# Performance work log

Hardware: AMD Instinct MI355X
Metric: run time of the kernel (lower is better)

## Reference

```python
import jax, jax.numpy as jnp
import numpy as np

B, N, C = 64, 8192, 64
C4 = C // 4
EPS_BN = 1e-5


def setup_inputs() -> dict:
    key = jax.random.key(0)
    ks = jax.random.split(key, 12)
    s = 0.05
    return {
        "x": jax.random.normal(ks[0], (B, N, 10), jnp.float32),
        "y": jax.random.normal(ks[1], (B, N, 13), jnp.float32),
        "W_l": jax.random.normal(ks[2], (10, C), jnp.float32) * s,
        "b_l": jax.random.normal(ks[3], (C,), jnp.float32) * s,
        "W_r": jax.random.normal(ks[4], (13, C), jnp.float32) * s,
        "b_r": jax.random.normal(ks[5], (C,), jnp.float32) * s,
        "W_qk": jax.random.normal(ks[6], (C4, C), jnp.float32) * s,  # shared q/k 1x1-conv weight
        "W_v": jax.random.normal(ks[7], (C, C), jnp.float32) * s,
        "b_v": jax.random.normal(ks[8], (C,), jnp.float32) * s,
        "W_t": jax.random.normal(ks[9], (C, C), jnp.float32) * s,
        "b_t": jax.random.normal(ks[10], (C,), jnp.float32) * s,
        "gamma": jnp.ones((C,), jnp.float32),
        "beta": jnp.zeros((C,), jnp.float32),
    }


def reference(x, y, W_l, b_l, W_r, b_r, W_qk, W_v, b_v, W_t, b_t, gamma, beta):
    # x: [B,N,10] -> linear_l; y: [B,N,13] -> linear_r  (torch keeps [B,C,N]; we keep [B,N,C])
    X = x @ W_l + b_l                                   # [B,N,C]
    Y = y @ W_r + b_r                                   # [B,N,C]
    # 1x1 convs == per-point matmuls; attention runs ACROSS the batch dim per point n
    xq = jnp.einsum('bnc,dc->nbd', X, W_qk)             # [N,B,C/4]
    yk = jnp.einsum('bnc,dc->nbd', Y, W_qk)             # [N,B,C/4] (shared weight)
    yv = jnp.einsum('bnc,dc->nbd', Y, W_v) + b_v        # [N,B,C]
    energy = jnp.einsum('nbd,ned->nbe', xq, yk)         # [N,B,B]
    attn = jax.nn.softmax(energy, axis=-1)
    # extra L1 renormalization over dim=1 (offset-attention style)
    attn = attn / (1e-9 + attn.sum(axis=1, keepdims=True))
    yr = jnp.einsum('nbe,nec->bnc', attn, yv)           # [B,N,C]
    # trans_conv -> BatchNorm (training-mode batch stats) -> ReLU -> residual -> max over points
    t = jnp.einsum('bnc,dc->bnd', X - yr, W_t) + b_t    # [B,N,C]
    mean = t.mean(axis=(0, 1))
    var = t.var(axis=(0, 1))                            # biased var, as BN uses
    tn = gamma * (t - mean) * jax.lax.rsqrt(var + EPS_BN) + beta
    xres = X + jax.nn.relu(tn)                          # [B,N,C]
    return jnp.max(xres, axis=1)[:, :, None]            # [B,C,1] to match torch layout
```

## Files before the change

kernel.cpp:

```cpp
#include <hip/hip_runtime.h>

#define B_ 64
#define N_ 8192

using short8 = __attribute__((ext_vector_type(8))) short;
using f32x4  = __attribute__((ext_vector_type(4))) float;

#define MFMA16(a, b, c) __builtin_amdgcn_mfma_f32_16x16x32_bf16((a), (b), (c), 0, 0, 0)

__device__ inline unsigned short f2bf(float f) {
  union { float f; unsigned int u; } v; v.f = f;
  return (unsigned short)((v.u + 0x8000u) >> 16);
}
__device__ inline float bf2f(unsigned int hi16_in_low) {
  union { unsigned int u; float f; } v; v.u = hi16_in_low << 16;
  return v.f;
}
__device__ inline unsigned u2(float a, float b) {
  return (unsigned)f2bf(a) | ((unsigned)f2bf(b) << 16);
}
__device__ inline void put_y(short* Ar0, short* YT0, int b, int f, unsigned short h) {
  const int s = (f >= 13) ? 1 : 0;
  Ar0[16 + f + 2547 * s] = (short)h;
  YT0[f * 72 + b + 216 * s] = (short)h;
}


__global__ void k0_prep(const float* __restrict__ W_l, const float* __restrict__ b_l,
                        const float* __restrict__ W_r, const float* __restrict__ b_r,
                        const float* __restrict__ W_qk, const float* __restrict__ W_v,
                        const float* __restrict__ b_v, const float* __restrict__ W_t,
                        float* __restrict__ wsf) {
  const int tid = threadIdx.x;
  unsigned short* wb   = (unsigned short*)(wsf + 66688);
  unsigned short* BM   = wb;
  unsigned short* BL   = wb + 512;
  unsigned short* BRV2 = wb + 2560;
  unsigned short* BT   = wb + 4608;
  if (blockIdx.x == 0) {
    __shared__ float Wlq[11 * 16], Wrk[14 * 16];
    for (int idx = tid; idx < 11 * 16; idx += 256) {
      int i = idx >> 4, d = idx & 15;
      const float* a = (i < 10) ? (W_l + i * 64) : b_l;
      float s = 0.f;
      for (int c = 0; c < 64; ++c) s = fmaf(a[c], W_qk[d * 64 + c], s);
      Wlq[idx] = s;
    }
    for (int idx = tid; idx < 14 * 16; idx += 256) {
      int j = idx >> 4, d = idx & 15;
      const float* a = (j < 13) ? (W_r + j * 64) : b_r;
      float s = 0.f;
      for (int c = 0; c < 64; ++c) s = fmaf(a[c], W_qk[d * 64 + c], s);
      Wrk[idx] = s;
    }
    __syncthreads();
    for (int idx = tid; idx < 512; idx += 256) {
      int j = idx >> 5, kk = idx & 31;
      unsigned short o = 0;
      if (j < 14 && kk < 11) {
        float s = 0.f;
        for (int d = 0; d < 16; ++d) s = fmaf(Wlq[kk * 16 + d], Wrk[j * 16 + d], s);
        o = f2bf(s);
      }
      BM[idx] = o;
    }
  } else if (blockIdx.x == 1) {
    for (int idx = tid; idx < 2048; idx += 256) {
      int c = idx >> 5, kk = idx & 31;
      unsigned short o = 0;
      if (kk < 13) {
        float s = 0.f;
        for (int j = 0; j < 64; ++j) s = fmaf(W_r[kk * 64 + j], W_v[c * 64 + j], s);
        o = f2bf(s);
      } else if (kk == 13) {
        float s = b_v[c];
        for (int j = 0; j < 64; ++j) s = fmaf(b_r[j], W_v[c * 64 + j], s);
        o = f2bf(s);
      }
      BRV2[idx] = o;
    }
  } else if (blockIdx.x == 2) {
    for (int idx = tid; idx < 2048; idx += 256) {
      int c = idx >> 5, kk = idx & 31;
      unsigned short o = 0;
      if (kk < 10) o = f2bf(W_l[kk * 64 + c]);
      else if (kk == 10) o = f2bf(b_l[c]);
      BL[idx] = o;
    }
    for (int i = tid; i < 1024; i += 256) wsf[i] = 0.f;
  } else {
    for (int i = tid; i < 4096; i += 256) BT[i] = f2bf(W_t[i]);
  }
}

__global__ __launch_bounds__(256, 4)
void k1_attn(const float* __restrict__ x, const float* __restrict__ y,
             const float* __restrict__ wsf, const float* __restrict__ b_t,
             float* __restrict__ stats) {
  __shared__ __align__(16) short lds[19712];
  float* const statsScr = (float*)lds;
  short* const Axy[2] = {lds, lds + 2560};
  short* const YTb[2] = {lds + 5120, lds + 6272};
  short* const awB    = lds + 7424;
  short* const guB    = lds + 16640;
  float* const csF    = (float*)(lds + 18688);

  const unsigned short* wb   = (const unsigned short*)(wsf + 66688);
  const unsigned short* BM   = wb;
  const unsigned short* BL   = wb + 512;
  const unsigned short* BRV2 = wb + 2560;
  const unsigned short* BT   = wb + 4608;
  unsigned short* tg = (unsigned short*)(wsf + 66688) + 8704;

  const int tid  = threadIdx.x;
  const int w    = tid >> 6;
  const int lane = tid & 63;
  const int l15  = lane & 15;
  const int q    = lane >> 4;
  const int r0   = w * 16;
  const int n0   = blockIdx.x * 2;
  short* const aw[2] = {awB + w * 1152, awB + (4 + w) * 1152};
  short* const gu[2] = {guB + w * 256,  guB + (4 + w) * 256};

  {
    const int b = tid >> 2, i = tid & 3;
    const float* xb = x + ((size_t)b * N_ + n0) * 10;
    const float* yb = y + ((size_t)b * N_ + n0) * 13;
    short* const Ar0 = Axy[0] + b * 40;
    short* const Ar1 = Axy[1] + b * 40;
    short* const YT0 = YTb[0];
    {
      const float4 v = *(const float4*)(xb + 4 * i);
      const int g0 = 4 * i, g1 = 4 * i + 2;
      *(unsigned*)(Ar0 + (g0 >= 10 ? g0 + 2550 : g0)) = u2(v.x, v.y);
      *(unsigned*)(Ar0 + (g1 >= 10 ? g1 + 2550 : g1)) = u2(v.z, v.w);
      if (i == 0) {
        const float4 vv = *(const float4*)(xb + 16);
        *(unsigned*)(Ar1 + 6) = u2(vv.x, vv.y);
        *(unsigned*)(Ar1 + 8) = u2(vv.z, vv.w);
      }
    }
    if (i == 1) { *(unsigned*)(Ar1 + 10) = 0x3F80u; *(unsigned*)(Ar1 + 12) = 0u; *(unsigned*)(Ar1 + 14) = 0u; }
    if (i == 2) { *(unsigned*)(Ar0 + 10) = 0x3F80u; *(unsigned*)(Ar0 + 12) = 0u; *(unsigned*)(Ar0 + 14) = 0u; }
#pragma unroll
    for (int t = 0; t < 3; ++t) {
      const int j = i + 4 * t;
      const float2 v = *(const float2*)(yb + 2 * j);
      put_y(Ar0, YT0, b, 2 * j,     f2bf(v.x));
      put_y(Ar0, YT0, b, 2 * j + 1, f2bf(v.y));
    }
    if (i == 0) {
      const float2 v = *(const float2*)(yb + 24);
      put_y(Ar0, YT0, b, 24, f2bf(v.x));
      put_y(Ar0, YT0, b, 25, f2bf(v.y));
    }
    if (i == 3) {
      Ar0[29] = (short)0x3F80; *(unsigned*)(Ar0 + 30) = 0u;
      YT0[13 * 72 + b] = (short)0x3F80; YT0[14 * 72 + b] = 0; YT0[15 * 72 + b] = 0;
    }
    if (i == 2) {
      Ar1[29] = (short)0x3F80; *(unsigned*)(Ar1 + 30) = 0u;
      short* YT1 = YT0 + 1152;
      YT1[13 * 72 + b] = (short)0x3F80; YT1[14 * 72 + b] = 0; YT1[15 * 72 + b] = 0;
    }
  }
  asm volatile("s_waitcnt lgkmcnt(0)" ::: "memory");
  __builtin_amdgcn_sched_barrier(0);

  const short8 z8 = {0, 0, 0, 0, 0, 0, 0, 0};
  const f32x4 zero4 = {0.f, 0.f, 0.f, 0.f};

  const short8 bmF = *(const short8*)&BM[l15 * 32 + q * 8];
  short8 blF[4];
#pragma unroll
  for (int f = 0; f < 4; ++f) blF[f] = *(const short8*)&BL[(f * 16 + l15) * 32 + q * 8];

  f32x4 X[2][4];
  __builtin_amdgcn_s_setprio(1);
#pragma unroll
  for (int p = 0; p < 2; ++p) {
    const short8 aA = *(const short8*)&Axy[p][(r0 + l15) * 40 + q * 8];
    f32x4 G = MFMA16(aA, bmF, zero4);
#pragma unroll
    for (int f = 0; f < 4; ++f) X[p][f] = MFMA16(aA, blF[f], zero4);
#pragma unroll
    for (int j = 0; j < 4; ++j) gu[p][(q * 4 + j) * 16 + l15] = (short)f2bf(G[j]);
  }
  __builtin_amdgcn_s_setprio(0);
  __syncthreads();

  f32x4 E[2][4];
  __builtin_amdgcn_s_setprio(1);
#pragma unroll
  for (int p = 0; p < 2; ++p) {
    short8 aG = z8;
    if (q < 2) aG = *(const short8*)&gu[p][l15 * 16 + q * 8];
#pragma unroll
    for (int f = 0; f < 4; ++f) {
      short8 bk = z8;
      if (q < 2) bk = *(const short8*)&Axy[p][(f * 16 + l15) * 40 + 16 + q * 8];
      E[p][f] = MFMA16(aG, bk, zero4);
    }
  }
  __builtin_amdgcn_s_setprio(0);

  float inv_r[2][4];
#pragma unroll
  for (int p = 0; p < 2; ++p)
#pragma unroll
    for (int j = 0; j < 4; ++j) {
      float s = 0.f;
#pragma unroll
      for (int f = 0; f < 4; ++f) { E[p][f][j] = __expf(E[p][f][j]); s += E[p][f][j]; }
      s += __shfl_xor(s, 1);
      s += __shfl_xor(s, 2);
      s += __shfl_xor(s, 4);
      s += __shfl_xor(s, 8);
      inv_r[p][j] = 1.0f / s;
    }
#pragma unroll
  for (int p = 0; p < 2; ++p)
#pragma unroll
    for (int f = 0; f < 4; ++f) {
      float cs = E[p][f][0] * inv_r[p][0] + E[p][f][1] * inv_r[p][1] +
                 E[p][f][2] * inv_r[p][2] + E[p][f][3] * inv_r[p][3];
      cs += __shfl_xor(cs, 16);
      cs += __shfl_xor(cs, 32);
      if (lane < 16) csF[p * 256 + w * 64 + f * 16 + l15] = cs;
    }
  __syncthreads();

#pragma unroll
  for (int p = 0; p < 2; ++p) {
#pragma unroll
    for (int f = 0; f < 4; ++f) {
      const int col = f * 16 + l15;
      const float* sp = csF + p * 256;
      const float csv = 1.0f / (1e-9f + sp[col] + sp[64 + col] + sp[128 + col] + sp[192 + col]);
#pragma unroll
      for (int j = 0; j < 4; ++j)
        aw[p][(q * 4 + j) * 72 + col] = (short)f2bf(E[p][f][j] * inv_r[p][j] * csv);
    }
  }

  short8 brvF[4];
#pragma unroll
  for (int f = 0; f < 4; ++f) brvF[f] = *(const short8*)&BRV2[(f * 16 + l15) * 32 + q * 8];
  __builtin_amdgcn_s_setprio(1);
#pragma unroll
  for (int p = 0; p < 2; ++p) {
    const short8 aA0 = *(const short8*)&aw[p][l15 * 72 + q * 8];
    const short8 aA1 = *(const short8*)&aw[p][l15 * 72 + 32 + q * 8];
    f32x4 U = MFMA16(aA0, *(const short8*)&YTb[p][l15 * 72 + q * 8], zero4);
    U = MFMA16(aA1, *(const short8*)&YTb[p][l15 * 72 + 32 + q * 8], U);
#pragma unroll
    for (int j = 0; j < 4; ++j) gu[p][(q * 4 + j) * 16 + l15] = (short)f2bf(U[j]);
    short8 aU = z8;
    if (q < 2) aU = *(const short8*)&gu[p][l15 * 16 + q * 8];
#pragma unroll
    for (int f = 0; f < 4; ++f) {
      f32x4 yr = MFMA16(aU, brvF[f], zero4);
#pragma unroll
      for (int j = 0; j < 4; ++j)
        aw[p][(q * 4 + j) * 72 + f * 16 + l15] = (short)f2bf(X[p][f][j] - yr[j]);
    }
  }
  __builtin_amdgcn_s_setprio(0);

  float sRed[2][4], ssRed[2][4];
  uint2 pk[2][4];
  float4 btv[4];
  short8 btF0[4], btF1[4];
#pragma unroll
  for (int f = 0; f < 4; ++f) {
    btv[f] = *(const float4*)&b_t[f * 16 + q * 4];
    const int c = f * 16 + l15;
    btF0[f] = *(const short8*)&BT[c * 64 + q * 8];
    btF1[f] = *(const short8*)&BT[c * 64 + 32 + q * 8];
  }
  __builtin_amdgcn_s_setprio(1);
#pragma unroll
  for (int p = 0; p < 2; ++p) {
    const short8 aZ0 = *(const short8*)&aw[p][l15 * 72 + q * 8];
    const short8 aZ1 = *(const short8*)&aw[p][l15 * 72 + 32 + q * 8];
#pragma unroll
    for (int f = 0; f < 4; ++f) {
      const int c = f * 16 + l15;
      const float bT = b_t[c];
      f32x4 t = MFMA16(aZ0, btF0[f], ((f32x4){bT, bT, bT, bT}));
      t = MFMA16(aZ1, btF1[f], t);
      float s = 0.f, ss = 0.f;
#pragma unroll
      for (int j = 0; j < 4; ++j) { s += t[j]; ss = fmaf(t[j], t[j], ss); }
      s  += __shfl_xor(s, 16);  s  += __shfl_xor(s, 32);
      ss += __shfl_xor(ss, 16); ss += __shfl_xor(ss, 32);
      sRed[p][f] = s; ssRed[p][f] = ss;
      f32x4 tc = MFMA16(btF0[f], aZ0, ((f32x4){btv[f].x, btv[f].y, btv[f].z, btv[f].w}));
      tc = MFMA16(btF1[f], aZ1, tc);
      pk[p][f].x = (unsigned)f2bf(tc[0]) | ((unsigned)f2bf(tc[1]) << 16);
      pk[p][f].y = (unsigned)f2bf(tc[2]) | ((unsigned)f2bf(tc[3]) << 16);
    }
  }
  __builtin_amdgcn_s_setprio(0);
#pragma unroll
  for (int p = 0; p < 2; ++p)
#pragma unroll
    for (int f = 0; f < 4; ++f)
      *(uint2*)&tg[(size_t)(n0 + p) * 4096 + (size_t)(r0 + l15) * 64 + f * 16 + q * 4] =
          pk[p][f];
#pragma unroll
  for (int p = 0; p < 2; ++p)
#pragma unroll
    for (int f = 0; f < 4; ++f)
      if (lane < 16) {
        statsScr[p * 512 + w * 64 + f * 16 + l15]       = sRed[p][f];
        statsScr[p * 512 + 256 + w * 64 + f * 16 + l15] = ssRed[p][f];
      }
  __syncthreads();
  if (tid < 128) {
    const int p = tid >> 6, c = tid & 63;
    const float* sp = statsScr + p * 512;
    const float s  = sp[c] + sp[64 + c] + sp[128 + c] + sp[192 + c];
    const float ss = sp[256 + c] + sp[320 + c] + sp[384 + c] + sp[448 + c];
    float* st = stats + ((n0 + p) & 7) * 128;
    atomicAdd(&st[c], s);
    atomicAdd(&st[64 + c], ss);
  }
}

__global__ __launch_bounds__(256)
void k3_max(const float* __restrict__ x, const float* __restrict__ W_l,
            const float* __restrict__ b_l, const float* __restrict__ gamma,
            const float* __restrict__ beta, const unsigned short* __restrict__ tg,
            const float* __restrict__ stats, float* __restrict__ pmax)
{
  const int b = blockIdx.x >> 4;
  const int chunk = blockIdx.x & 15;
  __shared__ __align__(16) float xs[512 * 10];
  __shared__ float mr[128];
  __shared__ float sm[4][64];
  {
    const float4* src = (const float4*)(x + ((size_t)b * N_ + (size_t)chunk * 512) * 10);
    float4* dst = (float4*)xs;
#pragma unroll
    for (int t = 0; t < 5; ++t) dst[threadIdx.x + 256 * t] = src[threadIdx.x + 256 * t];
  }
  if (threadIdx.x < 64) {
    const int c = threadIdx.x;
    float s = 0.f, ss = 0.f;
    for (int r = 0; r < 8; ++r) { s += stats[r * 128 + c]; ss += stats[r * 128 + 64 + c]; }
    const float inv = 1.0f / (float)(B_ * N_);
    const float mu = s * inv;
    const float var = fmaf(ss, inv, -mu * mu);
    mr[c] = mu;
    mr[64 + c] = rsqrtf(var + 1e-5f);
  }
  const int wv = threadIdx.x >> 6;
  const int lane = threadIdx.x & 63;
  const int c0 = (lane & 15) * 4;
  const int nsub = lane >> 4;
  float4 wl4[10];
#pragma unroll
  for (int k = 0; k < 10; ++k) wl4[k] = *(const float4*)&W_l[k * 64 + c0];
  const float4 bl  = *(const float4*)&b_l[c0];
  const float4 g   = *(const float4*)&gamma[c0];
  const float4 be  = *(const float4*)&beta[c0];
  __syncthreads();
  const float4 mu  = *(const float4*)&mr[c0];
  const float4 rs  = *(const float4*)&mr[64 + c0];
  float4 grs, bmb;
  grs.x = g.x * rs.x; grs.y = g.y * rs.y; grs.z = g.z * rs.z; grs.w = g.w * rs.w;
  bmb.x = be.x - mu.x * grs.x; bmb.y = be.y - mu.y * grs.y;
  bmb.z = be.z - mu.z * grs.z; bmb.w = be.w - mu.w * grs.w;
  float4 m = {-1e30f, -1e30f, -1e30f, -1e30f};
  const int ln0 = wv * 128 + nsub;
  const size_t tgbase = (size_t)(chunk * 512) * 4096 + (b << 6) + c0;
  uint2 tv[4];
#pragma unroll
  for (int u = 0; u < 4; ++u)
    tv[u] = *(const uint2*)&tg[tgbase + (size_t)(ln0 + u * 4) * 4096];
  for (int blk = 0; blk < 8; ++blk) {
    uint2 cur[4];
#pragma unroll
    for (int u = 0; u < 4; ++u) cur[u] = tv[u];
    if (blk < 7) {
#pragma unroll
      for (int u = 0; u < 4; ++u)
        tv[u] = *(const uint2*)&tg[tgbase + (size_t)(ln0 + (blk + 1) * 16 + u * 4) * 4096];
    }
#pragma unroll
    for (int u = 0; u < 4; ++u) {
      const int ln = ln0 + blk * 16 + u * 4;
      const float2* xr = (const float2*)(xs + ln * 10);
      float4 X = bl;
#pragma unroll
      for (int k = 0; k < 5; ++k) {
        const float2 xk = xr[k];
        X.x = fmaf(xk.x, wl4[2 * k].x, X.x); X.y = fmaf(xk.x, wl4[2 * k].y, X.y);
        X.z = fmaf(xk.x, wl4[2 * k].z, X.z); X.w = fmaf(xk.x, wl4[2 * k].w, X.w);
        X.x = fmaf(xk.y, wl4[2 * k + 1].x, X.x); X.y = fmaf(xk.y, wl4[2 * k + 1].y, X.y);
        X.z = fmaf(xk.y, wl4[2 * k + 1].z, X.z); X.w = fmaf(xk.y, wl4[2 * k + 1].w, X.w);
      }
      const float t0 = bf2f(cur[u].x & 0xFFFFu), t1 = bf2f(cur[u].x >> 16);
      const float t2 = bf2f(cur[u].y & 0xFFFFu), t3 = bf2f(cur[u].y >> 16);
      m.x = fmaxf(m.x, X.x + fmaxf(fmaf(t0, grs.x, bmb.x), 0.f));
      m.y = fmaxf(m.y, X.y + fmaxf(fmaf(t1, grs.y, bmb.y), 0.f));
      m.z = fmaxf(m.z, X.z + fmaxf(fmaf(t2, grs.z, bmb.z), 0.f));
      m.w = fmaxf(m.w, X.w + fmaxf(fmaf(t3, grs.w, bmb.w), 0.f));
    }
  }
  m.x = fmaxf(m.x, __shfl_xor(m.x, 16)); m.y = fmaxf(m.y, __shfl_xor(m.y, 16));
  m.z = fmaxf(m.z, __shfl_xor(m.z, 16)); m.w = fmaxf(m.w, __shfl_xor(m.w, 16));
  m.x = fmaxf(m.x, __shfl_xor(m.x, 32)); m.y = fmaxf(m.y, __shfl_xor(m.y, 32));
  m.z = fmaxf(m.z, __shfl_xor(m.z, 32)); m.w = fmaxf(m.w, __shfl_xor(m.w, 32));
  if (lane < 16) *(float4*)&sm[wv][c0] = m;
  __syncthreads();
  if (threadIdx.x < 64) {
    const float r = fmaxf(fmaxf(sm[0][threadIdx.x], sm[1][threadIdx.x]),
                          fmaxf(sm[2][threadIdx.x], sm[3][threadIdx.x]));
    pmax[(size_t)blockIdx.x * 64 + threadIdx.x] = r;
  }
}

__global__ void k4_final(const float* __restrict__ pmax, float* __restrict__ out) {
  const int b = blockIdx.x, c = threadIdx.x;
  float m = -1e30f;
  for (int ch = 0; ch < 16; ++ch) m = fmaxf(m, pmax[((size_t)b * 16 + ch) * 64 + c]);
  out[b * 64 + c] = m;
}

extern "C" void kernel_launch(void* const* d_in, const int* in_sizes, int n_in,
                              void* d_out, int out_size, void* d_ws, size_t ws_size,
                              hipStream_t stream) {
  const float* x     = (const float*)d_in[0];
  const float* y     = (const float*)d_in[1];
  const float* W_l   = (const float*)d_in[2];
  const float* b_l   = (const float*)d_in[3];
  const float* W_r   = (const float*)d_in[4];
  const float* b_r   = (const float*)d_in[5];
  const float* W_qk  = (const float*)d_in[6];
  const float* W_v   = (const float*)d_in[7];
  const float* b_v   = (const float*)d_in[8];
  const float* W_t   = (const float*)d_in[9];
  const float* b_t   = (const float*)d_in[10];
  const float* gamma = (const float*)d_in[11];
  const float* beta  = (const float*)d_in[12];
  float* out = (float*)d_out;

  float* wsf = (float*)d_ws;
  float* stats = wsf;
  float* pmax  = wsf + 1152;
  const unsigned short* tg = (const unsigned short*)(wsf + 66688) + 8704;

  hipLaunchKernelGGL(k0_prep, dim3(4), dim3(256), 0, stream,
                     W_l, b_l, W_r, b_r, W_qk, W_v, b_v, W_t, wsf);
  hipLaunchKernelGGL(k1_attn, dim3(N_ / 2), dim3(256), 0, stream,
                     x, y, wsf, b_t, stats);
  hipLaunchKernelGGL(k3_max, dim3(1024), dim3(256), 0, stream,
                     x, W_l, b_l, gamma, beta, tg, stats, pmax);
  hipLaunchKernelGGL(k4_final, dim3(64), dim3(64), 0, stream, pmax, out);
}
```

Before: 203.2 us.

## Fuse all stages into one cooperative persistent kernel with grid syncs

Refactors the prep, attention, max and final stages into device functions and runs them inside one cooperative kernel. Grid-wide syncs separate the stages, and blocks loop persistently over the virtual block indices. The goal is to remove the launch overhead and inter-kernel gaps of four separate launches. In exchange, occupancy is capped at 4 blocks per CU with a larger shared LDS footprint, and grid.sync adds its own cost. If the cooperative launch fails, the code falls back to the original four launches.

```diff
diff --git a/kernel.cpp b/kernel.cpp
--- a/kernel.cpp
+++ b/kernel.cpp
@@ -1,4 +1,7 @@
 #include <hip/hip_runtime.h>
+#include <hip/hip_cooperative_groups.h>
+
+namespace cg = cooperative_groups;
 
 #define B_ 64
 #define N_ 8192
@@ -26,19 +29,20 @@
 }
 
 
-__global__ void k0_prep(const float* __restrict__ W_l, const float* __restrict__ b_l,
-                        const float* __restrict__ W_r, const float* __restrict__ b_r,
-                        const float* __restrict__ W_qk, const float* __restrict__ W_v,
-                        const float* __restrict__ b_v, const float* __restrict__ W_t,
-                        float* __restrict__ wsf) {
-  const int tid = threadIdx.x;
+
+__device__ void prep_body(int bidx, int tid, float* smemf,
+                          const float* W_l, const float* b_l,
+                          const float* W_r, const float* b_r,
+                          const float* W_qk, const float* W_v,
+                          const float* b_v, const float* W_t, float* wsf) {
   unsigned short* wb   = (unsigned short*)(wsf + 66688);
   unsigned short* BM   = wb;
   unsigned short* BL   = wb + 512;
   unsigned short* BRV2 = wb + 2560;
   unsigned short* BT   = wb + 4608;
-  if (blockIdx.x == 0) {
-    __shared__ float Wlq[11 * 16], Wrk[14 * 16];
+  if (bidx == 0) {
+    float* Wlq = smemf;
+    float* Wrk = smemf + 176;
     for (int idx = tid; idx < 11 * 16; idx += 256) {
       int i = idx >> 4, d = idx & 15;
       const float* a = (i < 10) ? (W_l + i * 64) : b_l;
@@ -64,7 +68,7 @@
       }
       BM[idx] = o;
     }
-  } else if (blockIdx.x == 1) {
+  } else if (bidx == 1) {
     for (int idx = tid; idx < 2048; idx += 256) {
       int c = idx >> 5, kk = idx & 31;
       unsigned short o = 0;
@@ -79,7 +83,7 @@
       }
       BRV2[idx] = o;
     }
-  } else if (blockIdx.x == 2) {
+  } else if (bidx == 2) {
     for (int idx = tid; idx < 2048; idx += 256) {
       int c = idx >> 5, kk = idx & 31;
       unsigned short o = 0;
@@ -93,11 +97,10 @@
   }
 }
 
-__global__ __launch_bounds__(256, 4)
-void k1_attn(const float* __restrict__ x, const float* __restrict__ y,
-             const float* __restrict__ wsf, const float* __restrict__ b_t,
-             float* __restrict__ stats) {
-  __shared__ __align__(16) short lds[19712];
+__device__ void attn_body(int vb, int tid, short* lds,
+                          const float* __restrict__ x, const float* __restrict__ y,
+                          const float* __restrict__ wsf, const float* __restrict__ b_t,
+                          float* __restrict__ stats) {
   float* const statsScr = (float*)lds;
   short* const Axy[2] = {lds, lds + 2560};
   short* const YTb[2] = {lds + 5120, lds + 6272};
@@ -112,13 +115,12 @@
   const unsigned short* BT   = wb + 4608;
   unsigned short* tg = (unsigned short*)(wsf + 66688) + 8704;
 
-  const int tid  = threadIdx.x;
   const int w    = tid >> 6;
   const int lane = tid & 63;
   const int l15  = lane & 15;
   const int q    = lane >> 4;
   const int r0   = w * 16;
-  const int n0   = blockIdx.x * 2;
+  const int n0   = vb * 2;
   short* const aw[2] = {awB + w * 1152, awB + (4 + w) * 1152};
   short* const gu[2] = {guB + w * 256,  guB + (4 + w) * 256};
 
@@ -328,25 +330,24 @@
   }
 }
 
-__global__ __launch_bounds__(256)
-void k3_max(const float* __restrict__ x, const float* __restrict__ W_l,
-            const float* __restrict__ b_l, const float* __restrict__ gamma,
-            const float* __restrict__ beta, const unsigned short* __restrict__ tg,
-            const float* __restrict__ stats, float* __restrict__ pmax)
-{
-  const int b = blockIdx.x >> 4;
-  const int chunk = blockIdx.x & 15;
-  __shared__ __align__(16) float xs[512 * 10];
-  __shared__ float mr[128];
-  __shared__ float sm[4][64];
+__device__ void max_body(int vb, int tid, char* smem,
+                         const float* __restrict__ x, const float* __restrict__ W_l,
+                         const float* __restrict__ b_l, const float* __restrict__ gamma,
+                         const float* __restrict__ beta, const unsigned short* __restrict__ tg,
+                         const float* __restrict__ stats, float* __restrict__ pmax) {
+  const int b = vb >> 4;
+  const int chunk = vb & 15;
+  float* xs  = (float*)smem;
+  float* mr  = (float*)(smem + 20480);
+  float* smx = (float*)(smem + 20992);
   {
     const float4* src = (const float4*)(x + ((size_t)b * N_ + (size_t)chunk * 512) * 10);
     float4* dst = (float4*)xs;
 #pragma unroll
-    for (int t = 0; t < 5; ++t) dst[threadIdx.x + 256 * t] = src[threadIdx.x + 256 * t];
-  }
-  if (threadIdx.x < 64) {
-    const int c = threadIdx.x;
+    for (int t = 0; t < 5; ++t) dst[tid + 256 * t] = src[tid + 256 * t];
+  }
+  if (tid < 64) {
+    const int c = tid;
     float s = 0.f, ss = 0.f;
     for (int r = 0; r < 8; ++r) { s += stats[r * 128 + c]; ss += stats[r * 128 + 64 + c]; }
     const float inv = 1.0f / (float)(B_ * N_);
@@ -355,8 +356,8 @@
     mr[c] = mu;
     mr[64 + c] = rsqrtf(var + 1e-5f);
   }
-  const int wv = threadIdx.x >> 6;
-  const int lane = threadIdx.x & 63;
+  const int wv = tid >> 6;
+  const int lane = tid & 63;
   const int c0 = (lane & 15) * 4;
   const int nsub = lane >> 4;
   float4 wl4[10];
@@ -413,13 +414,76 @@
   m.z = fmaxf(m.z, __shfl_xor(m.z, 16)); m.w = fmaxf(m.w, __shfl_xor(m.w, 16));
   m.x = fmaxf(m.x, __shfl_xor(m.x, 32)); m.y = fmaxf(m.y, __shfl_xor(m.y, 32));
   m.z = fmaxf(m.z, __shfl_xor(m.z, 32)); m.w = fmaxf(m.w, __shfl_xor(m.w, 32));
-  if (lane < 16) *(float4*)&sm[wv][c0] = m;
+  if (lane < 16) *(float4*)&smx[wv * 64 + c0] = m;
   __syncthreads();
-  if (threadIdx.x < 64) {
-    const float r = fmaxf(fmaxf(sm[0][threadIdx.x], sm[1][threadIdx.x]),
-                          fmaxf(sm[2][threadIdx.x], sm[3][threadIdx.x]));
-    pmax[(size_t)blockIdx.x * 64 + threadIdx.x] = r;
-  }
+  if (tid < 64) {
+    const float r = fmaxf(fmaxf(smx[tid], smx[64 + tid]), fmaxf(smx[128 + tid], smx[192 + tid]));
+    pmax[(size_t)vb * 64 + tid] = r;
+  }
+}
+
+__global__ __launch_bounds__(256, 4)
+void mega(const float* __restrict__ x, const float* __restrict__ y,
+          const float* __restrict__ W_l, const float* __restrict__ b_l,
+          const float* __restrict__ W_r, const float* __restrict__ b_r,
+          const float* __restrict__ W_qk, const float* __restrict__ W_v,
+          const float* __restrict__ b_v, const float* __restrict__ W_t,
+          const float* __restrict__ b_t, const float* __restrict__ gamma,
+          const float* __restrict__ beta, float* __restrict__ wsf,
+          float* __restrict__ out) {
+  __shared__ __align__(16) char smem[39424];
+  const int tid = threadIdx.x;
+  float* stats = wsf;
+  float* pmax  = wsf + 1152;
+  const unsigned short* tg = (const unsigned short*)(wsf + 66688) + 8704;
+  cg::grid_group grid = cg::this_grid();
+
+  if (blockIdx.x < 4)
+    prep_body(blockIdx.x, tid, (float*)smem, W_l, b_l, W_r, b_r, W_qk, W_v, b_v, W_t, wsf);
+  grid.sync();
+
+  for (int vb = blockIdx.x; vb < N_ / 2; vb += gridDim.x) {
+    attn_body(vb, tid, (short*)smem, x, y, wsf, b_t, stats);
+    __syncthreads();
+  }
+  grid.sync();
+
+  for (int vb = blockIdx.x; vb < 1024; vb += gridDim.x)
+    max_body(vb, tid, smem, x, W_l, b_l, gamma, beta, tg, stats, pmax);
+  grid.sync();
+
+  if (blockIdx.x < 64 && tid < 64) {
+    const int b = blockIdx.x;
+    float m = -1e30f;
+    for (int ch = 0; ch < 16; ++ch) m = fmaxf(m, pmax[((size_t)b * 16 + ch) * 64 + tid]);
+    out[b * 64 + tid] = m;
+  }
+}
+
+__global__ void k0_prep(const float* __restrict__ W_l, const float* __restrict__ b_l,
+                        const float* __restrict__ W_r, const float* __restrict__ b_r,
+                        const float* __restrict__ W_qk, const float* __restrict__ W_v,
+                        const float* __restrict__ b_v, const float* __restrict__ W_t,
+                        float* __restrict__ wsf) {
+  __shared__ __align__(16) float sf[400];
+  prep_body(blockIdx.x, threadIdx.x, sf, W_l, b_l, W_r, b_r, W_qk, W_v, b_v, W_t, wsf);
+}
+
+__global__ __launch_bounds__(256, 4)
+void k1_attn(const float* __restrict__ x, const float* __restrict__ y,
+             const float* __restrict__ wsf, const float* __restrict__ b_t,
+             float* __restrict__ stats) {
+  __shared__ __align__(16) short lds[19712];
+  attn_body(blockIdx.x, threadIdx.x, lds, x, y, wsf, b_t, stats);
+}
+
+__global__ __launch_bounds__(256)
+void k3_max(const float* __restrict__ x, const float* __restrict__ W_l,
+            const float* __restrict__ b_l, const float* __restrict__ gamma,
+            const float* __restrict__ beta, const unsigned short* __restrict__ tg,
+            const float* __restrict__ stats, float* __restrict__ pmax) {
+  __shared__ __align__(16) char smem[22016];
+  max_body(blockIdx.x, threadIdx.x, smem, x, W_l, b_l, gamma, beta, tg, stats, pmax);
 }
 
 __global__ void k4_final(const float* __restrict__ pmax, float* __restrict__ out) {
@@ -446,12 +510,25 @@
   const float* gamma = (const float*)d_in[11];
   const float* beta  = (const float*)d_in[12];
   float* out = (float*)d_out;
-
   float* wsf = (float*)d_ws;
+
+  int nb = 0;
+  hipError_t qe = hipOccupancyMaxActiveBlocksPerMultiprocessor(&nb, (const void*)mega, 256, 0);
+  if (qe == hipSuccess && nb >= 1) {
+    if (nb > 4) nb = 4;
+    int gridn = nb * 256;
+    void* args[15] = {(void*)&x, (void*)&y, (void*)&W_l, (void*)&b_l, (void*)&W_r,
+                      (void*)&b_r, (void*)&W_qk, (void*)&W_v, (void*)&b_v, (void*)&W_t,
+                      (void*)&b_t, (void*)&gamma, (void*)&beta, (void*)&wsf, (void*)&out};
+    hipError_t le = hipLaunchCooperativeKernel((const void*)mega, dim3(gridn), dim3(256),
+                                               args, 0, stream);
+    if (le == hipSuccess) return;
+    (void)hipGetLastError();
+  }
+
   float* stats = wsf;
   float* pmax  = wsf + 1152;
   const unsigned short* tg = (const unsigned short*)(wsf + 66688) + 8704;
-
   hipLaunchKernelGGL(k0_prep, dim3(4), dim3(256), 0, stream,
                      W_l, b_l, W_r, b_r, W_qk, W_v, b_v, W_t, wsf);
   hipLaunchKernelGGL(k1_attn, dim3(N_ / 2), dim3(256), 0, stream,
```

New measurement: 471.7 us. 132% more time.

## Fuse final max into k3 via atomic keys and drop stats LDS reduction

Applied to the files above, without the earlier changes.

Replaces the block-level LDS reduction of BN statistics in the attention kernel with direct per-wave atomics spread over 16 slots, which removes a __syncthreads and LDS scratch. It also removes the separate final-max kernel: k3 applies atomicMax on order-preserving uint keys, and the last block, found with an atomic counter, decodes the keys into the output. The goal is to save one launch and a barrier. In exchange it adds more global atomic traffic and a threadfence.

```diff
diff --git a/kernel.cpp b/kernel.cpp
--- a/kernel.cpp
+++ b/kernel.cpp
@@ -18,6 +18,13 @@
 }
 __device__ inline unsigned u2(float a, float b) {
   return (unsigned)f2bf(a) | ((unsigned)f2bf(b) << 16);
+}
+__device__ inline unsigned fkey(float f) {
+  unsigned u = __float_as_uint(f);
+  return (u & 0x80000000u) ? ~u : (u | 0x80000000u);
+}
+__device__ inline float funkey(unsigned k) {
+  return (k & 0x80000000u) ? __uint_as_float(k ^ 0x80000000u) : __uint_as_float(~k);
 }
 __device__ inline void put_y(short* Ar0, short* YT0, int b, int f, unsigned short h) {
   const int s = (f >= 13) ? 1 : 0;
@@ -79,6 +86,8 @@
       }
       BRV2[idx] = o;
     }
+    unsigned* wu = (unsigned*)wsf;
+    for (int i = tid; i < 4097; i += 256) wu[2048 + i] = 0u;
   } else if (blockIdx.x == 2) {
     for (int idx = tid; idx < 2048; idx += 256) {
       int c = idx >> 5, kk = idx & 31;
@@ -87,7 +96,7 @@
       else if (kk == 10) o = f2bf(b_l[c]);
       BL[idx] = o;
     }
-    for (int i = tid; i < 1024; i += 256) wsf[i] = 0.f;
+    for (int i = tid; i < 2048; i += 256) wsf[i] = 0.f;
   } else {
     for (int i = tid; i < 4096; i += 256) BT[i] = f2bf(W_t[i]);
   }
@@ -98,7 +107,6 @@
              const float* __restrict__ wsf, const float* __restrict__ b_t,
              float* __restrict__ stats) {
   __shared__ __align__(16) short lds[19712];
-  float* const statsScr = (float*)lds;
   short* const Axy[2] = {lds, lds + 2560};
   short* const YTb[2] = {lds + 5120, lds + 6272};
   short* const awB    = lds + 7424;
@@ -308,23 +316,16 @@
     for (int f = 0; f < 4; ++f)
       *(uint2*)&tg[(size_t)(n0 + p) * 4096 + (size_t)(r0 + l15) * 64 + f * 16 + q * 4] =
           pk[p][f];
-#pragma unroll
-  for (int p = 0; p < 2; ++p)
-#pragma unroll
-    for (int f = 0; f < 4; ++f)
-      if (lane < 16) {
-        statsScr[p * 512 + w * 64 + f * 16 + l15]       = sRed[p][f];
-        statsScr[p * 512 + 256 + w * 64 + f * 16 + l15] = ssRed[p][f];
+  if (lane < 16) {
+#pragma unroll
+    for (int p = 0; p < 2; ++p) {
+      float* st = stats + ((n0 + p) & 15) * 128;
+#pragma unroll
+      for (int f = 0; f < 4; ++f) {
+        atomicAdd(&st[f * 16 + l15], sRed[p][f]);
+        atomicAdd(&st[64 + f * 16 + l15], ssRed[p][f]);
       }
-  __syncthreads();
-  if (tid < 128) {
-    const int p = tid >> 6, c = tid & 63;
-    const float* sp = statsScr + p * 512;
-    const float s  = sp[c] + sp[64 + c] + sp[128 + c] + sp[192 + c];
-    const float ss = sp[256 + c] + sp[320 + c] + sp[384 + c] + sp[448 + c];
-    float* st = stats + ((n0 + p) & 7) * 128;
-    atomicAdd(&st[c], s);
-    atomicAdd(&st[64 + c], ss);
+    }
   }
 }
 
@@ -332,13 +333,15 @@
 void k3_max(const float* __restrict__ x, const float* __restrict__ W_l,
             const float* __restrict__ b_l, const float* __restrict__ gamma,
             const float* __restrict__ beta, const unsigned short* __restrict__ tg,
-            const float* __restrict__ stats, float* __restrict__ pmax)
+            const float* __restrict__ stats, unsigned* __restrict__ keys,
+            unsigned* __restrict__ cnt, float* __restrict__ out)
 {
-  const int b = blockIdx.x >> 4;
-  const int chunk = blockIdx.x & 15;
+  const int b = blockIdx.x & 63;
+  const int chunk = blockIdx.x >> 6;
   __shared__ __align__(16) float xs[512 * 10];
   __shared__ float mr[128];
   __shared__ float sm[4][64];
+  __shared__ unsigned islast;
   {
     const float4* src = (const float4*)(x + ((size_t)b * N_ + (size_t)chunk * 512) * 10);
     float4* dst = (float4*)xs;
@@ -348,7 +351,7 @@
   if (threadIdx.x < 64) {
     const int c = threadIdx.x;
     float s = 0.f, ss = 0.f;
-    for (int r = 0; r < 8; ++r) { s += stats[r * 128 + c]; ss += stats[r * 128 + 64 + c]; }
+    for (int r = 0; r < 16; ++r) { s += stats[r * 128 + c]; ss += stats[r * 128 + 64 + c]; }
     const float inv = 1.0f / (float)(B_ * N_);
     const float mu = s * inv;
     const float var = fmaf(ss, inv, -mu * mu);
@@ -418,15 +421,18 @@
   if (threadIdx.x < 64) {
     const float r = fmaxf(fmaxf(sm[0][threadIdx.x], sm[1][threadIdx.x]),
                           fmaxf(sm[2][threadIdx.x], sm[3][threadIdx.x]));
-    pmax[(size_t)blockIdx.x * 64 + threadIdx.x] = r;
-  }
-}
-
-__global__ void k4_final(const float* __restrict__ pmax, float* __restrict__ out) {
-  const int b = blockIdx.x, c = threadIdx.x;
-  float m = -1e30f;
-  for (int ch = 0; ch < 16; ++ch) m = fmaxf(m, pmax[((size_t)b * 16 + ch) * 64 + c]);
-  out[b * 64 + c] = m;
+    atomicMax(&keys[b * 64 + threadIdx.x], fkey(r));
+  }
+  __threadfence();
+  if (threadIdx.x == 0)
+    islast = (atomicAdd(cnt, 1u) == (unsigned)(gridDim.x - 1)) ? 1u : 0u;
+  __syncthreads();
+  if (islast) {
+    for (int i = threadIdx.x; i < 4096; i += 256) {
+      const unsigned k = atomicOr(&keys[i], 0u);
+      out[i] = funkey(k);
+    }
+  }
 }
 
 extern "C" void kernel_launch(void* const* d_in, const int* in_sizes, int n_in,
@@ -449,7 +455,8 @@
 
   float* wsf = (float*)d_ws;
   float* stats = wsf;
-  float* pmax  = wsf + 1152;
+  unsigned* keys = (unsigned*)(wsf + 2048);
+  unsigned* cnt  = (unsigned*)(wsf + 6144);
   const unsigned short* tg = (const unsigned short*)(wsf + 66688) + 8704;
 
   hipLaunchKernelGGL(k0_prep, dim3(4), dim3(256), 0, stream,
@@ -457,6 +464,5 @@
   hipLaunchKernelGGL(k1_attn, dim3(N_ / 2), dim3(256), 0, stream,
                      x, y, wsf, b_t, stats);
   hipLaunchKernelGGL(k3_max, dim3(1024), dim3(256), 0, stream,
-                     x, W_l, b_l, gamma, beta, tg, stats, pmax);
-  hipLaunchKernelGGL(k4_final, dim3(64), dim3(64), 0, stream, pmax, out);
-}
+                     x, W_l, b_l, gamma, beta, tg, stats, keys, cnt, out);
+}
```

After: 301.7 us. 1.48x slower.

## Store X from attention kernel and stream BN-ReLU-max with atomic key reduction

Applied to the files above, without the earlier changes.

The attention kernel now also writes the projected X (as bf16) to workspace, computed by an extra transposed MFMA. A new streaming kernel reads t and X together, applies BN+ReLU+residual and max-reduces over points, then combines per-channel maxima across blocks via atomicMax on order-preserving float keys, with the last block writing the output. This replaces the previous max kernel, which recomputed X from x, and drops the separate final kernel. The cost is a larger workspace and an extra 64 MB bf16 write and read, and the path runs only when the workspace is large enough. X is now rounded to bf16, which slightly lowers precision.

```diff
diff --git a/kernel.cpp b/kernel.cpp
--- a/kernel.cpp
+++ b/kernel.cpp
@@ -18,6 +18,13 @@
 }
 __device__ inline unsigned u2(float a, float b) {
   return (unsigned)f2bf(a) | ((unsigned)f2bf(b) << 16);
+}
+__device__ inline unsigned fkey(float f) {
+  unsigned u = __float_as_uint(f);
+  return (u & 0x80000000u) ? ~u : (u | 0x80000000u);
+}
+__device__ inline float funkey(unsigned k) {
+  return (k & 0x80000000u) ? __uint_as_float(k ^ 0x80000000u) : __uint_as_float(~k);
 }
 __device__ inline void put_y(short* Ar0, short* YT0, int b, int f, unsigned short h) {
   const int s = (f >= 13) ? 1 : 0;
@@ -79,6 +86,8 @@
       }
       BRV2[idx] = o;
     }
+    unsigned* wu = (unsigned*)wsf;
+    for (int i = tid; i < 4097; i += 256) wu[2048 + i] = 0u;
   } else if (blockIdx.x == 2) {
     for (int idx = tid; idx < 2048; idx += 256) {
       int c = idx >> 5, kk = idx & 31;
@@ -96,7 +105,7 @@
 __global__ __launch_bounds__(256, 4)
 void k1_attn(const float* __restrict__ x, const float* __restrict__ y,
              const float* __restrict__ wsf, const float* __restrict__ b_t,
-             float* __restrict__ stats) {
+             float* __restrict__ stats, int writeX) {
   __shared__ __align__(16) short lds[19712];
   float* const statsScr = (float*)lds;
   short* const Axy[2] = {lds, lds + 2560};
@@ -111,6 +120,7 @@
   const unsigned short* BRV2 = wb + 2560;
   const unsigned short* BT   = wb + 4608;
   unsigned short* tg = (unsigned short*)(wsf + 66688) + 8704;
+  unsigned short* Xg = tg + (size_t)N_ * 4096;
 
   const int tid  = threadIdx.x;
   const int w    = tid >> 6;
@@ -185,6 +195,16 @@
     for (int f = 0; f < 4; ++f) X[p][f] = MFMA16(aA, blF[f], zero4);
 #pragma unroll
     for (int j = 0; j < 4; ++j) gu[p][(q * 4 + j) * 16 + l15] = (short)f2bf(G[j]);
+    if (writeX) {
+#pragma unroll
+      for (int f = 0; f < 4; ++f) {
+        f32x4 Xc = MFMA16(blF[f], aA, zero4);
+        uint2 xp2;
+        xp2.x = (unsigned)f2bf(Xc[0]) | ((unsigned)f2bf(Xc[1]) << 16);
+        xp2.y = (unsigned)f2bf(Xc[2]) | ((unsigned)f2bf(Xc[3]) << 16);
+        *(uint2*)&Xg[(size_t)(n0 + p) * 4096 + (size_t)(r0 + l15) * 64 + f * 16 + q * 4] = xp2;
+      }
+    }
   }
   __builtin_amdgcn_s_setprio(0);
   __syncthreads();
@@ -325,6 +345,72 @@
     float* st = stats + ((n0 + p) & 7) * 128;
     atomicAdd(&st[c], s);
     atomicAdd(&st[64 + c], ss);
+  }
+}
+
+__global__ __launch_bounds__(1024)
+void k3_stream(const unsigned short* __restrict__ tg, const unsigned short* __restrict__ Xg,
+               const float* __restrict__ stats, const float* __restrict__ gamma,
+               const float* __restrict__ beta, unsigned* __restrict__ keys,
+               unsigned* __restrict__ cnt, float* __restrict__ out)
+{
+  __shared__ float mr[128];
+  __shared__ float red[512 * 9];
+  __shared__ unsigned islast;
+  const int tid = threadIdx.x;
+  if (tid < 64) {
+    float s = 0.f, ss = 0.f;
+    for (int r = 0; r < 8; ++r) { s += stats[r * 128 + tid]; ss += stats[r * 128 + 64 + tid]; }
+    const float inv = 1.0f / (float)(B_ * N_);
+    const float mu = s * inv;
+    const float var = fmaf(ss, inv, -mu * mu);
+    mr[tid] = mu;
+    mr[64 + tid] = rsqrtf(var + 1e-5f);
+  }
+  __syncthreads();
+  const int c0 = (tid * 8) & 63;
+  float grs[8], bmb[8];
+#pragma unroll
+  for (int k = 0; k < 8; ++k) {
+    const float g = gamma[c0 + k], rs = mr[64 + c0 + k];
+    grs[k] = g * rs;
+    bmb[k] = beta[c0 + k] - mr[c0 + k] * grs[k];
+  }
+  const size_t base = (size_t)blockIdx.x * 32 * 4096 + (size_t)tid * 8;
+  float m[8];
+#pragma unroll
+  for (int k = 0; k < 8; ++k) m[k] = -1e30f;
+  for (int s = 0; s < 16; ++s) {
+    const size_t off = base + (size_t)s * 8192;
+    const uint4 tv = *(const uint4*)&tg[off];
+    const uint4 xv = *(const uint4*)&Xg[off];
+    const unsigned tw[4] = {tv.x, tv.y, tv.z, tv.w};
+    const unsigned xw[4] = {xv.x, xv.y, xv.z, xv.w};
+#pragma unroll
+    for (int u = 0; u < 4; ++u) {
+      const float t0 = bf2f(tw[u] & 0xFFFFu), t1 = bf2f(tw[u] >> 16);
+      const float x0 = bf2f(xw[u] & 0xFFFFu), x1 = bf2f(xw[u] >> 16);
+      m[2 * u]     = fmaxf(m[2 * u],     x0 + fmaxf(fmaf(t0, grs[2 * u],     bmb[2 * u]),     0.f));
+      m[2 * u + 1] = fmaxf(m[2 * u + 1], x1 + fmaxf(fmaf(t1, grs[2 * u + 1], bmb[2 * u + 1]), 0.f));
+    }
+  }
+  if (tid >= 512) {
+#pragma unroll
+    for (int k = 0; k < 8; ++k) red[(tid - 512) * 9 + k] = m[k];
+  }
+  __syncthreads();
+  if (tid < 512) {
+#pragma unroll
+    for (int k = 0; k < 8; ++k) {
+      const float v = fmaxf(m[k], red[tid * 9 + k]);
+      atomicMax(&keys[tid * 8 + k], fkey(v));
+    }
+  }
+  __threadfence();
+  if (tid == 0) islast = (atomicAdd(cnt, 1u) == (unsigned)(gridDim.x - 1)) ? 1u : 0u;
+  __syncthreads();
+  if (islast) {
+    for (int i = tid; i < 4096; i += 1024) out[i] = funkey(atomicOr(&keys[i], 0u));
   }
 }
 
@@ -449,14 +535,25 @@
 
   float* wsf = (float*)d_ws;
   float* stats = wsf;
-  float* pmax  = wsf + 1152;
+  unsigned* keys = (unsigned*)(wsf + 2048);
+  unsigned* cnt  = (unsigned*)(wsf + 6144);
+  float* pmax = wsf + 1152;
   const unsigned short* tg = (const unsigned short*)(wsf + 66688) + 8704;
+  const unsigned short* Xg = tg + (size_t)N_ * 4096;
+
+  const size_t need = 66688ull * 4 + 8704ull * 2 + 2ull * N_ * 4096 * 2;
+  const int streaming = (ws_size >= need) ? 1 : 0;
 
   hipLaunchKernelGGL(k0_prep, dim3(4), dim3(256), 0, stream,
                      W_l, b_l, W_r, b_r, W_qk, W_v, b_v, W_t, wsf);
   hipLaunchKernelGGL(k1_attn, dim3(N_ / 2), dim3(256), 0, stream,
-                     x, y, wsf, b_t, stats);
-  hipLaunchKernelGGL(k3_max, dim3(1024), dim3(256), 0, stream,
-                     x, W_l, b_l, gamma, beta, tg, stats, pmax);
-  hipLaunchKernelGGL(k4_final, dim3(64), dim3(64), 0, stream, pmax, out);
-}
+                     x, y, wsf, b_t, stats, streaming);
+  if (streaming) {
+    hipLaunchKernelGGL(k3_stream, dim3(256), dim3(1024), 0, stream,
+                       tg, Xg, stats, gamma, beta, keys, cnt, out);
+  } else {
+    hipLaunchKernelGGL(k3_max, dim3(1024), dim3(256), 0, stream,
+                       x, W_l, b_l, gamma, beta, tg, stats, pmax);
+    hipLaunchKernelGGL(k4_final, dim3(64), dim3(64), 0, stream, pmax, out);
+  }
+}
```

Result: slower. 307.5 us (+51.3%).
